# Performance work log

Hardware: AMD Instinct MI355X
Metric: run time of the kernel (lower is better)

The kernel has to match this reference:

```python
import jax, jax.numpy as jnp
import numpy as np

BINS = 10
VMIN = 0.0
VMAX = 1.0
SIGMA = 150.0
DELTA = (VMAX - VMIN) / BINS


def setup_inputs() -> dict:
    key = jax.random.key(0)
    kx, ky = jax.random.split(key)
    x = jax.random.uniform(kx, (16, 3, 512, 512), dtype=jnp.float32)
    y = jax.random.uniform(ky, (16, 3, 512, 512), dtype=jnp.float32)
    return {"x": x, "y": y}


def _soft_hist(img):
    # img: [B, 3, H, W] -> soft histogram [B, 3, BINS]
    centers = VMIN + DELTA * (jnp.arange(BINS, dtype=img.dtype) + 0.5)
    d = img[..., None] - centers  # [B, 3, H, W, BINS]
    w = jax.nn.sigmoid(SIGMA * (d + DELTA / 2)) - jax.nn.sigmoid(SIGMA * (d - DELTA / 2))
    return w.sum(axis=(2, 3))  # sum over all pixels


def reference(x, y):
    B = x.shape[0]
    hx = _soft_hist(x)  # [B, 3, BINS]
    hy = _soft_hist(y)
    # L1Loss (mean over bins) per (batch, channel), summed over batch and channels
    running = jnp.abs(hx - hy).mean(axis=-1).sum()
    return (running / B) * 0.0001
```

## Files before the change

kernel.cpp:

```cpp
#include <hip/hip_runtime.h>


static constexpr int PLANES   = 48;
static constexpr int PLANE_PX = 512 * 512;
static constexpr int SPP      = 16;
static constexpr int THREADS  = 256;
static constexpr int CHUNK    = PLANE_PX / SPP;
static constexpr int NBLK     = 96 * SPP;
static constexpr unsigned BASE = (255u << 18) + 1u;

__global__ __launch_bounds__(THREADS, 6) void soft_hist_partial(
    const float* __restrict__ xin, const float* __restrict__ yin,
    unsigned* __restrict__ G )
{
  __shared__ unsigned hist[11 * THREADS];
  __shared__ unsigned red[10 * 16 * 3];
  const int t = threadIdx.x;
  #pragma unroll
  for (int s = 0; s < 11; ++s) hist[s * THREADS + t] = 0u;
  __syncthreads();

  const int blk   = blockIdx.x;
  const int plane = blk >> 4;
  const int sub   = blk & 15;
  const float* src = (plane < PLANES ? xin + (size_t)plane * PLANE_PX
                                     : yin + (size_t)(plane - PLANES) * PLANE_PX)
                   + (size_t)sub * CHUNK;
  const float4* src4 = (const float4*)src;
  unsigned* mycol = hist + t;

  constexpr int ITERS = CHUNK / (THREADS * 4);
  float4 c0 = src4[t];
  float4 c1 = src4[THREADS + t];
  #pragma unroll 4
  for (int it = 0; it < ITERS; ++it) {
    float4 cur = c0;
    c0 = c1;
    if (it + 2 < ITERS) c1 = src4[(it + 2) * THREADS + t];
    float vv[4] = {cur.x, cur.y, cur.z, cur.w};
    #pragma unroll
    for (int j = 0; j < 4; ++j) {
      float W  = vv[j] * 10.0f;
      unsigned k = (unsigned)W;
      float d  = W - floorf(W);
      float mp = d - 0.5f;
      bool lo  = mp < 0.0f;
      float ex = __expf(fmaf(-15.0f, fabsf(mp), 7.5f));
      float sg = __builtin_amdgcn_rcpf(1.0f + ex);
      float scale = lo ? -255.0f : 62.0f;
      int   qs = (int)(sg * scale);
      unsigned sel = lo ? 18u : 7u;
      unsigned pk  = ((unsigned)qs << sel) + BASE;
      atomicAdd(&mycol[k << 8], pk);
    }
  }
  __syncthreads();

  if (t < 160) {
    const int bin = t >> 4, grp = t & 15;
    const uint4* hp = (const uint4*)(hist + (bin << 8) + (grp << 4));
    unsigned sa = 0, sb = 0, sc = 0;
    #pragma unroll
    for (int q = 0; q < 4; ++q) {
      uint4 u4 = hp[q];
      unsigned uu[4] = {u4.x, u4.y, u4.z, u4.w};
      #pragma unroll
      for (int e = 0; e < 4; ++e) {
        unsigned u = uu[e];
        sa += u >> 18; sb += (u >> 7) & 0x7FFu; sc += u & 0x7Fu;
      }
    }
    const int base = (bin * 16 + grp) * 3;
    red[base] = sa; red[base + 1] = sb; red[base + 2] = sc;
  }
  __syncthreads();

  if (t < 30) {
    const int bin = t / 3, c = t - 3 * bin;
    unsigned s = 0;
    #pragma unroll
    for (int g = 0; g < 16; ++g) s += red[(bin * 16 + g) * 3 + c];
    atomicAdd(&G[plane * 30 + bin * 3 + c], s);
  }
}

__global__ __launch_bounds__(512) void soft_hist_loss(
    const unsigned* __restrict__ G, float* __restrict__ out)
{
  __shared__ float wred[8];
  const int t = threadIdx.x;
  float val = 0.0f;
  if (t < 480) {
    const int pc = t / 10;
    const int i  = t - pc * 10;
    const unsigned* gx = G + pc * 30;
    const unsigned* gy = G + (pc + PLANES) * 30;
    float hx = (float)gx[3 * i] * (1.0f / 255.0f)
             - (float)gx[3 * i + 1] * (1.0f / 62.0f)
             + (i > 0 ? (float)gx[3 * (i - 1) + 1] * (1.0f / 62.0f) : 0.0f)
             + (i < 9 ? (float)gx[3 * (i + 1) + 2]
                      - (float)gx[3 * (i + 1)] * (1.0f / 255.0f) : 0.0f);
    float hy = (float)gy[3 * i] * (1.0f / 255.0f)
             - (float)gy[3 * i + 1] * (1.0f / 62.0f)
             + (i > 0 ? (float)gy[3 * (i - 1) + 1] * (1.0f / 62.0f) : 0.0f)
             + (i < 9 ? (float)gy[3 * (i + 1) + 2]
                      - (float)gy[3 * (i + 1)] * (1.0f / 255.0f) : 0.0f);
    val = fabsf(hx - hy);
  }
  #pragma unroll
  for (int off = 32; off >= 1; off >>= 1) val += __shfl_xor(val, off, 64);
  if ((t & 63) == 0) wred[t >> 6] = val;
  __syncthreads();
  if (t == 0) {
    float s = 0.0f;
    #pragma unroll
    for (int w = 0; w < 8; ++w) s += wred[w];
    out[0] = s * 6.25e-7f;
  }
}

extern "C" void kernel_launch(void* const* d_in, const int* in_sizes, int n_in,
                              void* d_out, int out_size, void* d_ws, size_t ws_size,
                              hipStream_t stream) {
  const float* x = (const float*)d_in[0];
  const float* y = (const float*)d_in[1];
  unsigned* G = (unsigned*)d_ws;
  hipMemsetAsync(d_ws, 0, 96 * 30 * sizeof(unsigned), stream);
  soft_hist_partial<<<NBLK, THREADS, 0, stream>>>(x, y, G);
  soft_hist_loss<<<1, 512, 0, stream>>>(G, (float*)d_out);
}
```

Before: 30.44 us.

## Bin pixels into fine count histogram and apply sigmoid weights per sub-bin

Replaces per-pixel exp/rcp soft-weight computation with a 2560-sub-bin integer count histogram in shared memory, then applies the sigmoid weights once per sub-bin in the epilogue and reduces with wave shuffles. This removes transcendental math from the per-pixel loop. In exchange, LDS atomics are now shared across threads with more contention, the sigmoid is approximated at sub-bin resolution, and the epilogue does more shuffle work.

```diff
diff --git a/kernel.cpp b/kernel.cpp
--- a/kernel.cpp
+++ b/kernel.cpp
@@ -7,17 +7,17 @@
 static constexpr int THREADS  = 256;
 static constexpr int CHUNK    = PLANE_PX / SPP;
 static constexpr int NBLK     = 96 * SPP;
-static constexpr unsigned BASE = (255u << 18) + 1u;
+static constexpr int HWORDS   = 5124;
+static constexpr float E15    = 3269017.3724721107f;
 
 __global__ __launch_bounds__(THREADS, 6) void soft_hist_partial(
     const float* __restrict__ xin, const float* __restrict__ yin,
     unsigned* __restrict__ G )
 {
-  __shared__ unsigned hist[11 * THREADS];
-  __shared__ unsigned red[10 * 16 * 3];
+  __shared__ unsigned hist[HWORDS];
+  __shared__ float fred[4][32];
   const int t = threadIdx.x;
-  #pragma unroll
-  for (int s = 0; s < 11; ++s) hist[s * THREADS + t] = 0u;
+  for (int i = t; i < HWORDS; i += THREADS) hist[i] = 0u;
   __syncthreads();
 
   const int blk   = blockIdx.x;
@@ -27,7 +27,7 @@
                                      : yin + (size_t)(plane - PLANES) * PLANE_PX)
                    + (size_t)sub * CHUNK;
   const float4* src4 = (const float4*)src;
-  unsigned* mycol = hist + t;
+  const unsigned col = (unsigned)(t & 1);
 
   constexpr int ITERS = CHUNK / (THREADS * 4);
   float4 c0 = src4[t];
@@ -39,48 +39,49 @@
     if (it + 2 < ITERS) c1 = src4[(it + 2) * THREADS + t];
     float vv[4] = {cur.x, cur.y, cur.z, cur.w};
     #pragma unroll
-    for (int j = 0; j < 4; ++j) {
-      float W  = vv[j] * 10.0f;
-      unsigned k = (unsigned)W;
-      float d  = W - floorf(W);
-      float mp = d - 0.5f;
-      bool lo  = mp < 0.0f;
-      float ex = __expf(fmaf(-15.0f, fabsf(mp), 7.5f));
-      float sg = __builtin_amdgcn_rcpf(1.0f + ex);
-      float scale = lo ? -255.0f : 62.0f;
-      int   qs = (int)(sg * scale);
-      unsigned sel = lo ? 18u : 7u;
-      unsigned pk  = ((unsigned)qs << sel) + BASE;
-      atomicAdd(&mycol[k << 8], pk);
+    for (int jj = 0; jj < 4; ++jj) {
+      unsigned j = (unsigned)(vv[jj] * 2560.0f);
+      atomicAdd(&hist[(j << 1) | col], 1u);
     }
   }
   __syncthreads();
 
-  if (t < 160) {
-    const int bin = t >> 4, grp = t & 15;
-    const uint4* hp = (const uint4*)(hist + (bin << 8) + (grp << 4));
-    unsigned sa = 0, sb = 0, sc = 0;
+  float dm = ((float)t + 0.5f) * (1.0f / 256.0f);
+  float ex = __expf(dm * -15.0f);
+  float wa = 1.0f / (1.0f + ex);
+  float wb = 1.0f / fmaf(E15, ex, 1.0f);
+
+  float pA[10], pB[10], pC[10];
+  #pragma unroll
+  for (int r = 0; r < 10; ++r) {
+    const int idx = ((r << 8) + t) << 1;
+    unsigned cn = hist[idx] + hist[idx | 1];
+    float cf = (float)cn;
+    pA[r] = wa * cf; pB[r] = wb * cf; pC[r] = cf;
+  }
+  #pragma unroll
+  for (int off = 32; off >= 1; off >>= 1) {
     #pragma unroll
-    for (int q = 0; q < 4; ++q) {
-      uint4 u4 = hp[q];
-      unsigned uu[4] = {u4.x, u4.y, u4.z, u4.w};
-      #pragma unroll
-      for (int e = 0; e < 4; ++e) {
-        unsigned u = uu[e];
-        sa += u >> 18; sb += (u >> 7) & 0x7FFu; sc += u & 0x7Fu;
-      }
+    for (int r = 0; r < 10; ++r) {
+      pA[r] += __shfl_xor(pA[r], off, 64);
+      pB[r] += __shfl_xor(pB[r], off, 64);
+      pC[r] += __shfl_xor(pC[r], off, 64);
     }
-    const int base = (bin * 16 + grp) * 3;
-    red[base] = sa; red[base + 1] = sb; red[base + 2] = sc;
+  }
+  const int lane = t & 63, w = t >> 6;
+  if (lane == 0) {
+    #pragma unroll
+    for (int r = 0; r < 10; ++r) {
+      fred[w][r * 3 + 0] = pA[r];
+      fred[w][r * 3 + 1] = pB[r];
+      fred[w][r * 3 + 2] = pC[r];
+    }
   }
   __syncthreads();
-
   if (t < 30) {
-    const int bin = t / 3, c = t - 3 * bin;
-    unsigned s = 0;
-    #pragma unroll
-    for (int g = 0; g < 16; ++g) s += red[(bin * 16 + g) * 3 + c];
-    atomicAdd(&G[plane * 30 + bin * 3 + c], s);
+    float s = fred[0][t] + fred[1][t] + fred[2][t] + fred[3][t];
+    unsigned q = (unsigned)fmaf(s, 64.0f, 0.5f);
+    atomicAdd(&G[plane * 30 + t], q);
   }
 }
 
@@ -95,16 +96,12 @@
     const int i  = t - pc * 10;
     const unsigned* gx = G + pc * 30;
     const unsigned* gy = G + (pc + PLANES) * 30;
-    float hx = (float)gx[3 * i] * (1.0f / 255.0f)
-             - (float)gx[3 * i + 1] * (1.0f / 62.0f)
-             + (i > 0 ? (float)gx[3 * (i - 1) + 1] * (1.0f / 62.0f) : 0.0f)
-             + (i < 9 ? (float)gx[3 * (i + 1) + 2]
-                      - (float)gx[3 * (i + 1)] * (1.0f / 255.0f) : 0.0f);
-    float hy = (float)gy[3 * i] * (1.0f / 255.0f)
-             - (float)gy[3 * i + 1] * (1.0f / 62.0f)
-             + (i > 0 ? (float)gy[3 * (i - 1) + 1] * (1.0f / 62.0f) : 0.0f)
-             + (i < 9 ? (float)gy[3 * (i + 1) + 2]
-                      - (float)gy[3 * (i + 1)] * (1.0f / 255.0f) : 0.0f);
+    float hx = (float)gx[3 * i] - (float)gx[3 * i + 1]
+             + (i > 0 ? (float)gx[3 * (i - 1) + 1] : 0.0f)
+             + (i < 9 ? (float)gx[3 * (i + 1) + 2] - (float)gx[3 * (i + 1)] : 0.0f);
+    float hy = (float)gy[3 * i] - (float)gy[3 * i + 1]
+             + (i > 0 ? (float)gy[3 * (i - 1) + 1] : 0.0f)
+             + (i < 9 ? (float)gy[3 * (i + 1) + 2] - (float)gy[3 * (i + 1)] : 0.0f);
     val = fabsf(hx - hy);
   }
   #pragma unroll
@@ -115,7 +112,7 @@
     float s = 0.0f;
     #pragma unroll
     for (int w = 0; w < 8; ++w) s += wred[w];
-    out[0] = s * 6.25e-7f;
+    out[0] = s * 9.765625e-9f;
   }
 }
 
```

Measured after the change: 39.77 us. 30.6% more time.
